# Kernel tuning notes

Hardware: AMD Instinct MI355X
Metric: run time of the kernel (lower is better)

Reference implementation:

```python
import jax, jax.numpy as jnp
import numpy as np

D_MODEL = 1024
N_HEADS = 16
D_K = D_MODEL // N_HEADS


def setup_inputs() -> dict:
    key = jax.random.key(0)
    k1, k2, k3 = jax.random.split(key, 3)
    x = jax.random.normal(k1, (4, 2048, D_MODEL), dtype=jnp.float32)
    # torch nn.Linear(d, 3d, bias=False): y = x @ W.T ; we store W.T directly as (in, out)
    w_qkv = jax.random.normal(k2, (D_MODEL, 3 * D_MODEL), dtype=jnp.float32) * (1.0 / np.sqrt(D_MODEL))
    w_out = jax.random.normal(k3, (D_MODEL, D_MODEL), dtype=jnp.float32) * (1.0 / np.sqrt(D_MODEL))
    return {"x": x, "w_qkv": w_qkv, "w_out": w_out}


def reference(x, w_qkv, w_out):
    B, T, D = x.shape
    qkv = jnp.einsum('btd,de->bte', x, w_qkv)  # (B,T,3D)
    q, k, v = jnp.split(qkv, 3, axis=-1)
    # split heads -> (B,H,T,d_k)
    def split_heads(t):
        return t.reshape(B, T, N_HEADS, D_K).transpose(0, 2, 1, 3)
    q, k, v = split_heads(q), split_heads(k), split_heads(v)
    scale = 1.0 / np.sqrt(D_K).astype(np.float32)
    scores = jnp.einsum('bhqd,bhkd->bhqk', q, k) * scale  # (B,H,T,T)
    causal = jnp.triu(jnp.full((T, T), -jnp.inf, dtype=scores.dtype), k=1)
    scores = scores + causal[None, None]
    weights = jax.nn.softmax(scores, axis=-1)
    attn = jnp.einsum('bhqk,bhkd->bhqd', weights, v)
    attn = attn.transpose(0, 2, 1, 3).reshape(B, T, D)
    return jnp.einsum('btd,de->bte', attn, w_out)
```

## Files before the change

kernel.cpp:

```cpp
#include <hip/hip_runtime.h>
#include <hip/hip_bf16.h>

typedef short short8 __attribute__((ext_vector_type(8)));
typedef float f32x4 __attribute__((ext_vector_type(4)));
typedef float f32x16 __attribute__((ext_vector_type(16)));

#define MFMA16(a, b, c) __builtin_amdgcn_mfma_f32_16x16x32_bf16((a), (b), (c), 0, 0, 0)
#define MFMA32(a, b, c) __builtin_amdgcn_mfma_f32_32x32x16_bf16((a), (b), (c), 0, 0, 0)

#define GLOAD16(gp, lp)                                                    \
    __builtin_amdgcn_global_load_lds(                                      \
        (const __attribute__((address_space(1))) unsigned int*)(gp),       \
        (__attribute__((address_space(3))) unsigned int*)(lp), 16, 0, 0)

__device__ __forceinline__ unsigned short f2b(float x) {
    unsigned int u = __float_as_uint(x);
    unsigned int r = u + 0x7FFFu + ((u >> 16) & 1u);
    return (unsigned short)(r >> 16);
}

#if __has_builtin(__builtin_amdgcn_cvt_pk_bf16_f32)
__device__ __forceinline__ unsigned pack2(float a, float b) {
    auto v = __builtin_amdgcn_cvt_pk_bf16_f32(a, b);
    unsigned u;
    __builtin_memcpy(&u, &v, 4);
    return u;
}
#else
__device__ __forceinline__ unsigned pack2(float a, float b) {
    return (unsigned)f2b(a) | ((unsigned)f2b(b) << 16);
}
#endif

__global__ __launch_bounds__(256) void cast4_kernel(const float* __restrict__ in,
                                                    unsigned short* __restrict__ out,
                                                    int n4) {
    int i = blockIdx.x * 256 + threadIdx.x;
    if (i < n4) {
        float4 v = ((const float4*)in)[i];
        ushort4 o;
        o.x = f2b(v.x); o.y = f2b(v.y); o.z = f2b(v.z); o.w = f2b(v.w);
        ((ushort4*)out)[i] = o;
    }
}

__global__ __launch_bounds__(256) void transpose_cast_f32(const float* __restrict__ in,
                                                          unsigned short* __restrict__ out,
                                                          int K, int N) {
    __shared__ unsigned short Ls[64 * 66];
    const int k0 = blockIdx.y * 64, n0 = blockIdx.x * 64;
    const int tid = threadIdx.x;
    const int krow = tid >> 4, nc4 = (tid & 15) * 4;
#pragma unroll
    for (int p = 0; p < 4; p++) {
        float4 v = *(const float4*)(in + (size_t)(k0 + krow + p * 16) * N + n0 + nc4);
        unsigned* d32 = (unsigned*)(Ls + (krow + p * 16) * 66 + nc4);
        d32[0] = pack2(v.x, v.y);
        d32[1] = pack2(v.z, v.w);
    }
    __syncthreads();
    const int n = tid >> 3, kc = (tid & 7) * 8;
#pragma unroll
    for (int p = 0; p < 2; p++) {
        int nn = n + p * 32;
        unsigned short w[8];
#pragma unroll
        for (int j = 0; j < 8; j++) w[j] = Ls[(kc + j) * 66 + nn];
        *(short8*)(out + (size_t)(n0 + nn) * K + k0 + kc) = *(short8*)w;
    }
}

__global__ __launch_bounds__(512, 2) void gemm_qkv(const unsigned short* __restrict__ A,
                                                   const unsigned short* __restrict__ Bt,
                                                   unsigned short* __restrict__ Qb,
                                                   unsigned short* __restrict__ Kb,
                                                   unsigned short* __restrict__ Vt) {
    __shared__ __align__(16) unsigned short smem[65536];

    const int tid  = threadIdx.x;
    const int wave = tid >> 6;
    const int lane = tid & 63;
    const int l32  = lane & 31;
    const int hi   = lane >> 5;
    const int wr   = wave >> 2;
    const int wc   = wave & 3;

    const int bid = blockIdx.x;
    const int sid = (bid & 7) * 48 + (bid >> 3);
    const int bx  = sid % 12;
    const int by  = sid / 12;
    const int m0 = by * 256;
    const int n0 = bx * 256;

    const int srow = tid >> 3;
    const int cswz = (((tid & 7) ^ ((tid >> 3) & 7)) * 8);
    const unsigned short* gA = A  + (size_t)(m0 + srow) * 1024 + cswz;
    const unsigned short* gB = Bt + (size_t)(n0 + srow) * 1024 + cswz;

#define STAGE_A(buf, h, kt) do {                                              \
        const unsigned short* _g = gA + (size_t)((h) * 128) * 1024 + (kt) * 64; \
        unsigned short* _l = smem + (buf) * 16384 + (h) * 8192 + wave * 512;  \
        GLOAD16(_g, _l);                                                      \
        GLOAD16(_g + 65536, _l + 4096);                                       \
    } while (0)
#define STAGE_B(buf, h, kt) do {                                              \
        const unsigned short* _g = gB + (size_t)((h) * 128) * 1024 + (kt) * 64; \
        unsigned short* _l = smem + 32768 + (buf) * 16384 + (h) * 8192 + wave * 512; \
        GLOAD16(_g, _l);                                                      \
        GLOAD16(_g + 65536, _l + 4096);                                       \
    } while (0)

    const int sw7  = l32 & 7;
    const int aoff = (wr * 128 + l32) * 64;
    const int boff = (wc * 64 + l32) * 64;

    f32x16 acc[4][2] = {};

    STAGE_A(0, 0, 0); STAGE_A(0, 1, 0); STAGE_B(0, 0, 0); STAGE_B(0, 1, 0);
    STAGE_B(1, 0, 1); STAGE_B(1, 1, 1); STAGE_A(1, 0, 1);
    asm volatile("s_waitcnt vmcnt(6)" ::: "memory");
    __builtin_amdgcn_s_barrier();

#pragma unroll
    for (int t = 0; t < 16; ++t) {
        const int b = t & 1;
        const unsigned short* Ab = smem + b * 16384;
        const unsigned short* Bb = smem + 32768 + b * 16384;

        short8 afLo[2][4], afHi[2][4], bf0[4], bf1[4];

#pragma unroll
        for (int rf = 0; rf < 2; ++rf)
#pragma unroll
            for (int ks = 0; ks < 4; ++ks)
                afLo[rf][ks] = *(const short8*)(Ab + aoff + rf * 2048 + (((ks * 2 + hi) ^ sw7) * 8));
#pragma unroll
        for (int ks = 0; ks < 4; ++ks)
            bf0[ks] = *(const short8*)(Bb + boff + (((ks * 2 + hi) ^ sw7) * 8));
        if (t + 1 < 16) STAGE_A(b ^ 1, 1, t + 1);
        __builtin_amdgcn_s_barrier();
        asm volatile("s_waitcnt lgkmcnt(0)" ::: "memory");
        __builtin_amdgcn_s_setprio(1);
#pragma unroll
        for (int ks = 0; ks < 4; ++ks) {
            acc[0][0] = MFMA32(afLo[0][ks], bf0[ks], acc[0][0]);
            acc[1][0] = MFMA32(afLo[1][ks], bf0[ks], acc[1][0]);
        }
        __builtin_amdgcn_s_setprio(0);
        __builtin_amdgcn_s_barrier();

#pragma unroll
        for (int ks = 0; ks < 4; ++ks)
            bf1[ks] = *(const short8*)(Bb + boff + 2048 + (((ks * 2 + hi) ^ sw7) * 8));
        __builtin_amdgcn_s_barrier();
        asm volatile("s_waitcnt lgkmcnt(0)" ::: "memory");
        __builtin_amdgcn_s_setprio(1);
#pragma unroll
        for (int ks = 0; ks < 4; ++ks) {
            acc[0][1] = MFMA32(afLo[0][ks], bf1[ks], acc[0][1]);
            acc[1][1] = MFMA32(afLo[1][ks], bf1[ks], acc[1][1]);
        }
        __builtin_amdgcn_s_setprio(0);
        __builtin_amdgcn_s_barrier();

#pragma unroll
        for (int rf = 0; rf < 2; ++rf)
#pragma unroll
            for (int ks = 0; ks < 4; ++ks)
                afHi[rf][ks] = *(const short8*)(Ab + aoff + (2 + rf) * 2048 + (((ks * 2 + hi) ^ sw7) * 8));
        if (t + 2 < 16) { STAGE_B(b, 0, t + 2); STAGE_B(b, 1, t + 2); }
        __builtin_amdgcn_s_barrier();
        asm volatile("s_waitcnt lgkmcnt(0)" ::: "memory");
        __builtin_amdgcn_s_setprio(1);
#pragma unroll
        for (int ks = 0; ks < 4; ++ks) {
            acc[2][0] = MFMA32(afHi[0][ks], bf0[ks], acc[2][0]);
            acc[3][0] = MFMA32(afHi[1][ks], bf0[ks], acc[3][0]);
        }
        __builtin_amdgcn_s_setprio(0);
        __builtin_amdgcn_s_barrier();

        if (t + 2 < 16) {
            STAGE_A(b, 0, t + 2);
            asm volatile("s_waitcnt vmcnt(6)" ::: "memory");
        } else {
            asm volatile("s_waitcnt vmcnt(0)" ::: "memory");
        }
        __builtin_amdgcn_s_barrier();
        __builtin_amdgcn_s_setprio(1);
#pragma unroll
        for (int ks = 0; ks < 4; ++ks) {
            acc[2][1] = MFMA32(afHi[0][ks], bf1[ks], acc[2][1]);
            acc[3][1] = MFMA32(afHi[1][ks], bf1[ks], acc[3][1]);
        }
        __builtin_amdgcn_s_setprio(0);
        __builtin_amdgcn_s_barrier();
    }
#undef STAGE_A
#undef STAGE_B

    if (n0 < 2048) {
        unsigned short* outp = (n0 < 1024) ? Qb : Kb;
        const int cb = (n0 < 1024) ? n0 : n0 - 1024;
        const float QS = (n0 < 1024) ? 0.125f * 1.44269504f : 1.0f;
#pragma unroll
        for (int rf = 0; rf < 4; ++rf)
#pragma unroll
            for (int cf = 0; cf < 2; ++cf)
#pragma unroll
                for (int r = 0; r < 16; ++r) {
                    int row = m0 + wr * 128 + rf * 32 + (r & 3) + 8 * (r >> 2) + 4 * hi;
                    int col = cb + wc * 64 + cf * 32 + l32;
                    outp[(size_t)row * 1024 + col] = f2b(acc[rf][cf][r] * QS);
                }
    } else {
        const int bb = m0 >> 11, t0b = m0 & 2047;
        const int hbase = (n0 - 2048) >> 6;
        unsigned short* reg = smem + wc * 16384;
#pragma unroll
        for (int rf = 0; rf < 4; ++rf)
#pragma unroll
            for (int cf = 0; cf < 2; ++cf)
#pragma unroll
                for (int rg = 0; rg < 4; ++rg) {
                    const int tl = wr * 128 + rf * 32 + rg * 8 + 4 * hi;
                    const int d  = cf * 32 + l32;
                    const int w  = d * 128 + ((tl >> 1) ^ (4 * (d & 7)));
                    uint2 v;
                    v.x = pack2(acc[rf][cf][4 * rg + 0], acc[rf][cf][4 * rg + 1]);
                    v.y = pack2(acc[rf][cf][4 * rg + 2], acc[rf][cf][4 * rg + 3]);
                    *(uint2*)(reg + 2 * w) = v;
                }
        __syncthreads();
#pragma unroll
        for (int it = 0; it < 16; ++it) {
            const int id = it * 512 + tid;
            const int hh = id >> 11, d = (id >> 5) & 63, k = id & 31;
            const int kb = k >> 2, kl = k & 3;
            const int xx = 4 * (d & 7);
            const unsigned short* bp = smem + hh * 16384 + 2 * (d * 128);
            uint2 lo  = *(const uint2*)(bp + 2 * ((16 * kb + 2 * kl) ^ xx));
            uint2 hi2 = *(const uint2*)(bp + 2 * ((16 * kb + 2 * kl + 8) ^ xx));
            uint2 parts[2] = {lo, hi2};
            short8 v; __builtin_memcpy(&v, parts, 16);
            *(short8*)(Vt + ((size_t)((bb * 16 + hbase + hh) * 64 + d)) * 2048 + t0b + k * 8) = v;
        }
    }
}

__global__ __launch_bounds__(256) void gemm_out(const unsigned short* __restrict__ A,
                                                const unsigned short* __restrict__ Bt,
                                                float* __restrict__ C) {
    const int K = 1024, lda = 1024;
    __shared__ unsigned short As[64 * 32];
    __shared__ unsigned short Bs[128 * 32];

    const int tid  = threadIdx.x;
    const int wave = tid >> 6;
    const int lane = tid & 63;
    const int l32  = lane & 31;
    const int hi   = lane >> 5;
    const int m0 = blockIdx.y * 64;
    const int n0 = blockIdx.x * 128;
    const int wm = (wave >> 1) * 32;
    const int wn = (wave & 1) * 64;

    const int srow = lane >> 2;
    const int scol = (((lane & 3) ^ ((lane >> 3) & 3)) * 8);
    const int fsw  = ((l32 >> 1) & 3);

    const unsigned short* Ag  = A  + (size_t)(m0 + wave * 16 + srow) * lda + scol;
    const unsigned short* Bg0 = Bt + (size_t)(n0 + wave * 32 + srow)      * K + scol;
    const unsigned short* Bg1 = Bt + (size_t)(n0 + wave * 32 + 16 + srow) * K + scol;
    unsigned short* Al  = As + wave * 512;
    unsigned short* Bl0 = Bs + (wave * 2 + 0) * 512;
    unsigned short* Bl1 = Bs + (wave * 2 + 1) * 512;

    f32x16 acc[2] = {};

    for (int k0 = 0; k0 < K; k0 += 32) {
        __syncthreads();
        GLOAD16(Ag + k0, Al);
        GLOAD16(Bg0 + k0, Bl0);
        GLOAD16(Bg1 + k0, Bl1);
        __syncthreads();

        short8 af[2], bf[2][2];
        {
            const int row = wm + l32;
#pragma unroll
            for (int ks = 0; ks < 2; ks++)
                af[ks] = *(const short8*)(As + row * 32 + ((ks * 2 + hi) ^ fsw) * 8);
        }
#pragma unroll
        for (int j = 0; j < 2; j++) {
            const int row = wn + j * 32 + l32;
#pragma unroll
            for (int ks = 0; ks < 2; ks++)
                bf[j][ks] = *(const short8*)(Bs + row * 32 + ((ks * 2 + hi) ^ fsw) * 8);
        }
#pragma unroll
        for (int ks = 0; ks < 2; ks++)
#pragma unroll
            for (int j = 0; j < 2; j++)
                acc[j] = MFMA32(af[ks], bf[j][ks], acc[j]);
    }

#pragma unroll
    for (int j = 0; j < 2; j++)
#pragma unroll
        for (int r = 0; r < 16; r++) {
            int row = m0 + wm + (r & 3) + 8 * (r >> 2) + 4 * hi;
            int col = n0 + wn + j * 32 + l32;
            C[(size_t)row * 1024 + col] = acc[j][r];
        }
}

__global__ __launch_bounds__(256) void attention_kernel(const unsigned short* Qb,
                                                        const unsigned short* Kb,
                                                        const unsigned short* Vt,
                                                        unsigned short* attn) {
    const int T = 2048;
    const int bi = blockIdx.x;
    const int qb = 31 - (bi >> 6);
    const int hb = bi & 63;
    const int b = hb >> 4, h = hb & 15;
    const int qb0 = qb * 64;
    const int tid = threadIdx.x, wave = tid >> 6, lane = tid & 63;
    const int l16 = lane & 15, quad = lane >> 4;
    const int qw0 = qb0 + wave * 16;

    const unsigned short* Qp  = Qb + (size_t)b * T * 1024 + h * 64;
    const unsigned short* Kp  = Kb + (size_t)b * T * 1024 + h * 64;
    const unsigned short* Vbh = Vt + ((size_t)(b * 16 + h) * 64) * 2048;

    __shared__ unsigned short Ks[2][64 * 32];
    __shared__ unsigned short Vts[2][64 * 32];

    short8 qf[2];
#pragma unroll
    for (int kd = 0; kd < 2; kd++)
        qf[kd] = *(const short8*)(Qp + (size_t)(qw0 + l16) * 1024 + kd * 32 + quad * 8);

    f32x4 o[4] = {};
    f32x4 o_l = {};
    const f32x4 fz = {};

    short8 onesf;
#pragma unroll
    for (int e = 0; e < 8; e++) onesf[e] = (short)0x3F80;

    const int srow = lane >> 2;
    const int scol = (((lane & 3) ^ ((lane >> 3) & 3)) * 8);
    const int sw8  = ((l16 >> 1) & 3) * 8;
    const size_t ktstep = (wave < 2) ? (size_t)64 * 1024 : (size_t)64;
    const size_t cstep  = (wave < 2) ? (size_t)16 * 1024 : (size_t)16 * T;
    const unsigned short* g0 = (wave < 2)
            ? Kp + (size_t)srow * 1024 + wave * 32 + scol
            : Vbh + (size_t)srow * T + (wave - 2) * 32 + scol;
    unsigned short* l0 = (wave < 2) ? Ks[wave] : Vts[wave - 2];

    for (int kt = 0; kt <= qb; kt++) {
        const int tk0 = kt * 64;
        const unsigned short* g = g0 + (size_t)kt * ktstep;
        __syncthreads();
#pragma unroll
        for (int c = 0; c < 4; c++) GLOAD16(g + c * cstep, l0 + c * 512);
        __syncthreads();

#pragma unroll
        for (int th = 0; th < 2; th++) {
            const int t0a = tk0 + th * 64 / 2;
            if (t0a > qw0 + 15) continue;
            const int t1 = t0a + 16;
            const bool act1 = (t1 <= qw0 + 15);

            f32x4 s0, s1;
            {
                const int row = (th * 2) * 16 + l16;
                short8 kf0 = *(const short8*)(Ks[0] + row * 32 + (quad * 8 ^ sw8));
                short8 kf1 = *(const short8*)(Ks[1] + row * 32 + (quad * 8 ^ sw8));
                s0 = MFMA16(kf0, qf[0], fz);
                s0 = MFMA16(kf1, qf[1], s0);
            }
            if (act1) {
                const int row = (th * 2 + 1) * 16 + l16;
                short8 kf0 = *(const short8*)(Ks[0] + row * 32 + (quad * 8 ^ sw8));
                short8 kf1 = *(const short8*)(Ks[1] + row * 32 + (quad * 8 ^ sw8));
                s1 = MFMA16(kf0, qf[0], fz);
                s1 = MFMA16(kf1, qf[1], s1);
            }

            unsigned u00, u01, u10, u11;
            {
                const bool full = (t0a + 15) <= qw0;
                float p[4];
#pragma unroll
                for (int r = 0; r < 4; r++) {
                    float e = __builtin_amdgcn_exp2f(s0[r]);
                    if (!full)
                        e = (t0a + quad * 4 + r <= qw0 + l16) ? e : 0.f;
                    p[r] = e;
                }
                u00 = pack2(p[0], p[1]);
                u01 = pack2(p[2], p[3]);
            }
            if (act1) {
                const bool full = (t1 + 15) <= qw0;
                float p[4];
#pragma unroll
                for (int r = 0; r < 4; r++) {
                    float e = __builtin_amdgcn_exp2f(s1[r]);
                    if (!full)
                        e = (t1 + quad * 4 + r <= qw0 + l16) ? e : 0.f;
                    p[r] = e;
                }
                u10 = pack2(p[0], p[1]);
                u11 = pack2(p[2], p[3]);
            } else {
                u10 = 0; u11 = 0;
            }

            unsigned pb[4] = {u00, u01, u10, u11};
            short8 pf; __builtin_memcpy(&pf, pb, 16);

            o_l = MFMA16(onesf, pf, o_l);
#pragma unroll
            for (int dt = 0; dt < 4; dt++) {
                short8 vf = *(const short8*)(Vts[th] + (dt * 16 + l16) * 32 + (quad * 8 ^ sw8));
                o[dt] = MFMA16(vf, pf, o[dt]);
            }
        }
    }

    const float rl = 1.f / o_l[0];
    const int q = qw0 + l16;
#pragma unroll
    for (int dt = 0; dt < 4; dt++) {
        ushort4 wv;
        wv.x = f2b(o[dt][0] * rl);
        wv.y = f2b(o[dt][1] * rl);
        wv.z = f2b(o[dt][2] * rl);
        wv.w = f2b(o[dt][3] * rl);
        *(ushort4*)(attn + (size_t)(b * T + q) * 1024 + h * 64 + dt * 16 + quad * 4) = wv;
    }
}

extern "C" void kernel_launch(void* const* d_in, const int* in_sizes, int n_in,
                              void* d_out, int out_size, void* d_ws, size_t ws_size,
                              hipStream_t stream) {
    const float* x     = (const float*)d_in[0];
    const float* w_qkv = (const float*)d_in[1];
    const float* w_out = (const float*)d_in[2];
    float* out = (float*)d_out;

    const int M = 8192, D = 1024, E = 3072;
    const size_t MB = 1048576;

    char* ws = (char*)d_ws;
    unsigned short* xb    = (unsigned short*)ws;
    unsigned short* wqkvT = (unsigned short*)(ws + 16 * MB);
    unsigned short* woutT = (unsigned short*)(ws + 22 * MB);
    unsigned short* Qb    = (unsigned short*)(ws + 24 * MB);
    unsigned short* Kb    = (unsigned short*)(ws + 40 * MB);
    unsigned short* Vt    = (unsigned short*)(ws + 56 * MB);

    cast4_kernel<<<M * D / 4 / 256, 256, 0, stream>>>(x, xb, M * D / 4);
    transpose_cast_f32<<<dim3(E / 64, D / 64), 256, 0, stream>>>(w_qkv, wqkvT, D, E);
    transpose_cast_f32<<<dim3(D / 64, D / 64), 256, 0, stream>>>(w_out, woutT, D, D);

    gemm_qkv<<<dim3(384), 512, 0, stream>>>(xb, wqkvT, Qb, Kb, Vt);

    attention_kernel<<<dim3(2048), 256, 0, stream>>>(Qb, Kb, Vt, Qb);

    gemm_out<<<dim3(D / 128, M / 64), 256, 0, stream>>>(Qb, woutT, out);
}
```

Baseline: 255.9 us.

## Pipeline output GEMM with larger tiles and double-buffer attention K/V loads

The output projection GEMM becomes a 512-thread, 128x256-tile kernel. It double-buffers LDS staging, interleaves async global-to-LDS loads with MFMA phases under explicit waitcnt and barriers, raises MFMA priority with setprio, and remaps block IDs for cache locality. The attention kernel moves to 512-thread blocks covering 128 queries and double-buffers K/V tiles, so the next tile's loads overlap compute instead of sitting between two syncthreads. This targets load latency exposed by the old single-buffered loops, but relies on hand-counted vmcnt values and larger LDS and register use, which may reduce occupancy.

```diff
diff --git a/kernel.cpp b/kernel.cpp
--- a/kernel.cpp
+++ b/kernel.cpp
@@ -248,99 +248,156 @@
     }
 }
 
-__global__ __launch_bounds__(256) void gemm_out(const unsigned short* __restrict__ A,
-                                                const unsigned short* __restrict__ Bt,
-                                                float* __restrict__ C) {
-    const int K = 1024, lda = 1024;
-    __shared__ unsigned short As[64 * 32];
-    __shared__ unsigned short Bs[128 * 32];
+__global__ __launch_bounds__(512, 2) void gemm_out(const unsigned short* __restrict__ A,
+                                                   const unsigned short* __restrict__ Bt,
+                                                   float* __restrict__ C) {
+    __shared__ __align__(16) unsigned short smem[49152];
 
     const int tid  = threadIdx.x;
     const int wave = tid >> 6;
     const int lane = tid & 63;
     const int l32  = lane & 31;
     const int hi   = lane >> 5;
-    const int m0 = blockIdx.y * 64;
-    const int n0 = blockIdx.x * 128;
-    const int wm = (wave >> 1) * 32;
-    const int wn = (wave & 1) * 64;
-
-    const int srow = lane >> 2;
-    const int scol = (((lane & 3) ^ ((lane >> 3) & 3)) * 8);
-    const int fsw  = ((l32 >> 1) & 3);
-
-    const unsigned short* Ag  = A  + (size_t)(m0 + wave * 16 + srow) * lda + scol;
-    const unsigned short* Bg0 = Bt + (size_t)(n0 + wave * 32 + srow)      * K + scol;
-    const unsigned short* Bg1 = Bt + (size_t)(n0 + wave * 32 + 16 + srow) * K + scol;
-    unsigned short* Al  = As + wave * 512;
-    unsigned short* Bl0 = Bs + (wave * 2 + 0) * 512;
-    unsigned short* Bl1 = Bs + (wave * 2 + 1) * 512;
-
-    f32x16 acc[2] = {};
-
-    for (int k0 = 0; k0 < K; k0 += 32) {
-        __syncthreads();
-        GLOAD16(Ag + k0, Al);
-        GLOAD16(Bg0 + k0, Bl0);
-        GLOAD16(Bg1 + k0, Bl1);
-        __syncthreads();
-
-        short8 af[2], bf[2][2];
-        {
-            const int row = wm + l32;
-#pragma unroll
-            for (int ks = 0; ks < 2; ks++)
-                af[ks] = *(const short8*)(As + row * 32 + ((ks * 2 + hi) ^ fsw) * 8);
-        }
-#pragma unroll
-        for (int j = 0; j < 2; j++) {
-            const int row = wn + j * 32 + l32;
-#pragma unroll
-            for (int ks = 0; ks < 2; ks++)
-                bf[j][ks] = *(const short8*)(Bs + row * 32 + ((ks * 2 + hi) ^ fsw) * 8);
-        }
-#pragma unroll
-        for (int ks = 0; ks < 2; ks++)
-#pragma unroll
-            for (int j = 0; j < 2; j++)
-                acc[j] = MFMA32(af[ks], bf[j][ks], acc[j]);
-    }
-
-#pragma unroll
-    for (int j = 0; j < 2; j++)
-#pragma unroll
-        for (int r = 0; r < 16; r++) {
-            int row = m0 + wm + (r & 3) + 8 * (r >> 2) + 4 * hi;
-            int col = n0 + wn + j * 32 + l32;
-            C[(size_t)row * 1024 + col] = acc[j][r];
-        }
-}
-
-__global__ __launch_bounds__(256) void attention_kernel(const unsigned short* Qb,
-                                                        const unsigned short* Kb,
-                                                        const unsigned short* Vt,
-                                                        unsigned short* attn) {
+    const int wr   = wave >> 2;
+    const int wc   = wave & 3;
+
+    const int bid = blockIdx.x;
+    const int sid = (bid & 7) * 32 + (bid >> 3);
+    const int bx  = sid & 3;
+    const int by  = sid >> 2;
+    const int m0 = by * 128;
+    const int n0 = bx * 256;
+
+    const int srow = tid >> 3;
+    const int cswz = (((tid & 7) ^ ((tid >> 3) & 7)) * 8);
+    const unsigned short* gA = A  + (size_t)(m0 + srow) * 1024 + cswz;
+    const unsigned short* gB = Bt + (size_t)(n0 + srow) * 1024 + cswz;
+
+#define STAGE_A(buf, h, kt) do {                                              \
+        const unsigned short* _g = gA + (size_t)((h) * 64) * 1024 + (kt) * 64; \
+        unsigned short* _l = smem + (buf) * 8192 + (h) * 4096 + wave * 512;   \
+        GLOAD16(_g, _l);                                                      \
+    } while (0)
+#define STAGE_B(buf, h, kt) do {                                              \
+        const unsigned short* _g = gB + (size_t)((h) * 128) * 1024 + (kt) * 64; \
+        unsigned short* _l = smem + 16384 + (buf) * 16384 + (h) * 8192 + wave * 512; \
+        GLOAD16(_g, _l);                                                      \
+        GLOAD16(_g + 65536, _l + 4096);                                       \
+    } while (0)
+
+    const int sw7  = l32 & 7;
+    const int aoff = (wr * 64 + l32) * 64;
+    const int boff = (wc * 64 + l32) * 64;
+
+    f32x16 acc[2][2] = {};
+
+    STAGE_A(0, 0, 0); STAGE_A(0, 1, 0); STAGE_B(0, 0, 0); STAGE_B(0, 1, 0);
+    STAGE_B(1, 0, 1); STAGE_B(1, 1, 1); STAGE_A(1, 0, 1);
+    asm volatile("s_waitcnt vmcnt(5)" ::: "memory");
+    __builtin_amdgcn_s_barrier();
+
+#pragma unroll
+    for (int t = 0; t < 16; ++t) {
+        const int b = t & 1;
+        const unsigned short* Ab = smem + b * 8192;
+        const unsigned short* Bb = smem + 16384 + b * 16384;
+
+        short8 af0[4], af1[4], bf0[4], bf1[4];
+
+#pragma unroll
+        for (int ks = 0; ks < 4; ++ks)
+            af0[ks] = *(const short8*)(Ab + aoff + (((ks * 2 + hi) ^ sw7) * 8));
+#pragma unroll
+        for (int ks = 0; ks < 4; ++ks)
+            bf0[ks] = *(const short8*)(Bb + boff + (((ks * 2 + hi) ^ sw7) * 8));
+        if (t + 1 < 16) STAGE_A(b ^ 1, 1, t + 1);
+        __builtin_amdgcn_s_barrier();
+        asm volatile("s_waitcnt lgkmcnt(0)" ::: "memory");
+        __builtin_amdgcn_s_setprio(1);
+#pragma unroll
+        for (int ks = 0; ks < 4; ++ks)
+            acc[0][0] = MFMA32(af0[ks], bf0[ks], acc[0][0]);
+        __builtin_amdgcn_s_setprio(0);
+        __builtin_amdgcn_s_barrier();
+
+#pragma unroll
+        for (int ks = 0; ks < 4; ++ks)
+            bf1[ks] = *(const short8*)(Bb + boff + 2048 + (((ks * 2 + hi) ^ sw7) * 8));
+        __builtin_amdgcn_s_barrier();
+        asm volatile("s_waitcnt lgkmcnt(0)" ::: "memory");
+        __builtin_amdgcn_s_setprio(1);
+#pragma unroll
+        for (int ks = 0; ks < 4; ++ks)
+            acc[0][1] = MFMA32(af0[ks], bf1[ks], acc[0][1]);
+        __builtin_amdgcn_s_setprio(0);
+        __builtin_amdgcn_s_barrier();
+
+#pragma unroll
+        for (int ks = 0; ks < 4; ++ks)
+            af1[ks] = *(const short8*)(Ab + aoff + 2048 + (((ks * 2 + hi) ^ sw7) * 8));
+        if (t + 2 < 16) { STAGE_B(b, 0, t + 2); STAGE_B(b, 1, t + 2); }
+        __builtin_amdgcn_s_barrier();
+        asm volatile("s_waitcnt lgkmcnt(0)" ::: "memory");
+        __builtin_amdgcn_s_setprio(1);
+#pragma unroll
+        for (int ks = 0; ks < 4; ++ks)
+            acc[1][0] = MFMA32(af1[ks], bf0[ks], acc[1][0]);
+        __builtin_amdgcn_s_setprio(0);
+        __builtin_amdgcn_s_barrier();
+
+        if (t + 2 < 16) {
+            STAGE_A(b, 0, t + 2);
+            asm volatile("s_waitcnt vmcnt(5)" ::: "memory");
+        } else {
+            asm volatile("s_waitcnt vmcnt(0)" ::: "memory");
+        }
+        __builtin_amdgcn_s_barrier();
+        __builtin_amdgcn_s_setprio(1);
+#pragma unroll
+        for (int ks = 0; ks < 4; ++ks)
+            acc[1][1] = MFMA32(af1[ks], bf1[ks], acc[1][1]);
+        __builtin_amdgcn_s_setprio(0);
+        __builtin_amdgcn_s_barrier();
+    }
+#undef STAGE_A
+#undef STAGE_B
+
+#pragma unroll
+    for (int rf = 0; rf < 2; ++rf)
+#pragma unroll
+        for (int cf = 0; cf < 2; ++cf)
+#pragma unroll
+            for (int r = 0; r < 16; ++r) {
+                int row = m0 + wr * 64 + rf * 32 + (r & 3) + 8 * (r >> 2) + 4 * hi;
+                int col = n0 + wc * 64 + cf * 32 + l32;
+                C[(size_t)row * 1024 + col] = acc[rf][cf][r];
+            }
+}
+
+__global__ __launch_bounds__(512, 8) void attention_kernel(const unsigned short* Qb,
+                                                           const unsigned short* Kb,
+                                                           const unsigned short* Vt,
+                                                           unsigned short* attn) {
     const int T = 2048;
     const int bi = blockIdx.x;
-    const int qb = 31 - (bi >> 6);
+    const int qb = 15 - (bi >> 6);
     const int hb = bi & 63;
     const int b = hb >> 4, h = hb & 15;
-    const int qb0 = qb * 64;
     const int tid = threadIdx.x, wave = tid >> 6, lane = tid & 63;
     const int l16 = lane & 15, quad = lane >> 4;
-    const int qw0 = qb0 + wave * 16;
+    const int qw0 = qb * 128 + wave * 16;
 
     const unsigned short* Qp  = Qb + (size_t)b * T * 1024 + h * 64;
     const unsigned short* Kp  = Kb + (size_t)b * T * 1024 + h * 64;
     const unsigned short* Vbh = Vt + ((size_t)(b * 16 + h) * 64) * 2048;
 
-    __shared__ unsigned short Ks[2][64 * 32];
-    __shared__ unsigned short Vts[2][64 * 32];
+    __shared__ __align__(16) unsigned short smem[2][8192];
 
     short8 qf[2];
 #pragma unroll
     for (int kd = 0; kd < 2; kd++)
         qf[kd] = *(const short8*)(Qp + (size_t)(qw0 + l16) * 1024 + kd * 32 + quad * 8);
+    asm volatile("" ::: "memory");
 
     f32x4 o[4] = {};
     f32x4 o_l = {};
@@ -353,24 +410,50 @@
     const int srow = lane >> 2;
     const int scol = (((lane & 3) ^ ((lane >> 3) & 3)) * 8);
     const int sw8  = ((l16 >> 1) & 3) * 8;
-    const size_t ktstep = (wave < 2) ? (size_t)64 * 1024 : (size_t)64;
-    const size_t cstep  = (wave < 2) ? (size_t)16 * 1024 : (size_t)16 * T;
-    const unsigned short* g0 = (wave < 2)
-            ? Kp + (size_t)srow * 1024 + wave * 32 + scol
-            : Vbh + (size_t)srow * T + (wave - 2) * 32 + scol;
-    unsigned short* l0 = (wave < 2) ? Ks[wave] : Vts[wave - 2];
-
-    for (int kt = 0; kt <= qb; kt++) {
+
+    const unsigned short* gs;
+    size_t ktstep, jstep;
+    int lofs;
+    if (wave < 4) {
+        const int p = wave >> 1, cp = wave & 1;
+        gs = Kp + (size_t)(cp * 32 + srow) * 1024 + p * 32 + scol;
+        ktstep = (size_t)64 * 1024; jstep = (size_t)16 * 1024;
+        lofs = p * 2048 + cp * 1024;
+    } else {
+        const int u = wave - 4, th = u >> 1, cp = u & 1;
+        gs = Vbh + (size_t)(cp * 32 + srow) * 2048 + th * 32 + scol;
+        ktstep = (size_t)64; jstep = (size_t)16 * 2048;
+        lofs = 4096 + th * 2048 + cp * 1024;
+    }
+
+#define STAGE(bb, kt) do {                                   \
+        const unsigned short* _g = gs + (size_t)(kt) * ktstep; \
+        unsigned short* _l = &smem[bb][0] + lofs;             \
+        GLOAD16(_g, _l);                                      \
+        GLOAD16(_g + jstep, _l + 512);                        \
+    } while (0)
+
+    STAGE(0, 0);
+    const int last = 2 * qb + 1;
+    for (int kt = 0; kt <= last; kt++) {
+        const int bsel = kt & 1;
         const int tk0 = kt * 64;
-        const unsigned short* g = g0 + (size_t)kt * ktstep;
-        __syncthreads();
-#pragma unroll
-        for (int c = 0; c < 4; c++) GLOAD16(g + c * cstep, l0 + c * 512);
-        __syncthreads();
+        if (kt < last) {
+            STAGE(bsel ^ 1, kt + 1);
+            asm volatile("s_waitcnt vmcnt(2)" ::: "memory");
+        } else {
+            asm volatile("s_waitcnt vmcnt(0)" ::: "memory");
+        }
+        __builtin_amdgcn_s_barrier();
+        asm volatile("" ::: "memory");
+
+        const unsigned short* Kb0 = &smem[bsel][0];
+        const unsigned short* Kb1 = Kb0 + 2048;
+        const unsigned short* Vb0 = Kb0 + 4096;
 
 #pragma unroll
         for (int th = 0; th < 2; th++) {
-            const int t0a = tk0 + th * 64 / 2;
+            const int t0a = tk0 + th * 32;
             if (t0a > qw0 + 15) continue;
             const int t1 = t0a + 16;
             const bool act1 = (t1 <= qw0 + 15);
@@ -378,15 +461,15 @@
             f32x4 s0, s1;
             {
                 const int row = (th * 2) * 16 + l16;
-                short8 kf0 = *(const short8*)(Ks[0] + row * 32 + (quad * 8 ^ sw8));
-                short8 kf1 = *(const short8*)(Ks[1] + row * 32 + (quad * 8 ^ sw8));
+                short8 kf0 = *(const short8*)(Kb0 + row * 32 + (quad * 8 ^ sw8));
+                short8 kf1 = *(const short8*)(Kb1 + row * 32 + (quad * 8 ^ sw8));
                 s0 = MFMA16(kf0, qf[0], fz);
                 s0 = MFMA16(kf1, qf[1], s0);
             }
             if (act1) {
                 const int row = (th * 2 + 1) * 16 + l16;
-                short8 kf0 = *(const short8*)(Ks[0] + row * 32 + (quad * 8 ^ sw8));
-                short8 kf1 = *(const short8*)(Ks[1] + row * 32 + (quad * 8 ^ sw8));
+                short8 kf0 = *(const short8*)(Kb0 + row * 32 + (quad * 8 ^ sw8));
+                short8 kf1 = *(const short8*)(Kb1 + row * 32 + (quad * 8 ^ sw8));
                 s1 = MFMA16(kf0, qf[0], fz);
                 s1 = MFMA16(kf1, qf[1], s1);
             }
@@ -424,14 +507,19 @@
             unsigned pb[4] = {u00, u01, u10, u11};
             short8 pf; __builtin_memcpy(&pf, pb, 16);
 
+            __builtin_amdgcn_s_setprio(1);
             o_l = MFMA16(onesf, pf, o_l);
 #pragma unroll
             for (int dt = 0; dt < 4; dt++) {
-                short8 vf = *(const short8*)(Vts[th] + (dt * 16 + l16) * 32 + (quad * 8 ^ sw8));
+                short8 vf = *(const short8*)(Vb0 + th * 2048 + (dt * 16 + l16) * 32 + (quad * 8 ^ sw8));
                 o[dt] = MFMA16(vf, pf, o[dt]);
             }
-        }
-    }
+            __builtin_amdgcn_s_setprio(0);
+        }
+        asm volatile("" ::: "memory");
+        __builtin_amdgcn_s_barrier();
+    }
+#undef STAGE
 
     const float rl = 1.f / o_l[0];
     const int q = qw0 + l16;
@@ -471,7 +559,7 @@
 
     gemm_qkv<<<dim3(384), 512, 0, stream>>>(xb, wqkvT, Qb, Kb, Vt);
 
-    attention_kernel<<<dim3(2048), 256, 0, stream>>>(Qb, Kb, Vt, Qb);
-
-    gemm_out<<<dim3(D / 128, M / 64), 256, 0, stream>>>(Qb, woutT, out);
-}
+    attention_kernel<<<dim3(1024), 512, 0, stream>>>(Qb, Kb, Vt, Qb);
+
+    gemm_out<<<dim3(256), 512, 0, stream>>>(Qb, woutT, out);
+}
```

Result: faster. 248.3 us (-3.0%).
